# Kernel tuning notes

Hardware: AMD Instinct MI355X
Metric: run time of the kernel (lower is better)

Reference implementation:

```python
import jax, jax.numpy as jnp
import numpy as np

B, T, D, H, L, V = 2, 1024, 768, 12, 6, 32000
HD = D // H
EPS = 1e-5


def _ln(x, w, b):
    mu = jnp.mean(x, axis=-1, keepdims=True)
    var = jnp.mean((x - mu) ** 2, axis=-1, keepdims=True)
    return (x - mu) * jax.lax.rsqrt(var + EPS) * w + b


def setup_inputs() -> dict:
    key = jax.random.key(0)
    ks = jax.random.split(key, 20)
    s = 0.02
    inp = {
        "idx": jax.random.randint(ks[0], (B, T), 0, V),
        "wte": jax.random.normal(ks[1], (V, D), jnp.float32) * s,
        "wpe": jax.random.normal(ks[2], (T, D), jnp.float32) * s,
        # per-layer stacked params (leading dim L)
        "ln1_w": jnp.ones((L, D), jnp.float32),
        "ln1_b": jnp.zeros((L, D), jnp.float32),
        "attn_w": jax.random.normal(ks[3], (L, D, 3 * D), jnp.float32) * s,
        "attn_b": jnp.zeros((L, 3 * D), jnp.float32),
        "proj_w": jax.random.normal(ks[4], (L, D, D), jnp.float32) * s,
        "proj_b": jnp.zeros((L, D), jnp.float32),
        "ln2_w": jnp.ones((L, D), jnp.float32),
        "ln2_b": jnp.zeros((L, D), jnp.float32),
        "fc_w": jax.random.normal(ks[5], (L, D, 4 * D), jnp.float32) * s,
        "fc_b": jnp.zeros((L, 4 * D), jnp.float32),
        "fcproj_w": jax.random.normal(ks[6], (L, 4 * D, D), jnp.float32) * s,
        "fcproj_b": jnp.zeros((L, D), jnp.float32),
        "lnf_w": jnp.ones((D,), jnp.float32),
        "lnf_b": jnp.zeros((D,), jnp.float32),
        "head_w": jax.random.normal(ks[7], (D, V), jnp.float32) * s,
    }
    return inp


def _forward(idx, wte, wpe, ln1_w, ln1_b, attn_w, attn_b, proj_w, proj_b,
             ln2_w, ln2_b, fc_w, fc_b, fcproj_w, fcproj_b, lnf_w, lnf_b, head_w):
    t = idx.shape[1]
    x = wte[idx] + wpe[:t][None]  # [B,T,D]
    causal = jnp.tril(jnp.ones((t, t), bool))
    neg_inf = jnp.asarray(-jnp.inf, x.dtype)
    scale = 1.0 / np.sqrt(HD)

    def block(x, p):
        l1w, l1b, aw, ab, pw, pb, l2w, l2b, fw, fb, fpw, fpb = p
        h = _ln(x, l1w, l1b)
        qkv = h @ aw + ab  # [B,T,3D]
        q, k, v = jnp.split(qkv, 3, axis=-1)
        q = q.reshape(B, t, H, HD).transpose(0, 2, 1, 3)
        k = k.reshape(B, t, H, HD).transpose(0, 2, 1, 3)
        v = v.reshape(B, t, H, HD).transpose(0, 2, 1, 3)
        att = jnp.einsum('bhqd,bhkd->bhqk', q, k) * scale
        att = jnp.where(causal, att, neg_inf)
        att = jax.nn.softmax(att, axis=-1)
        y = jnp.einsum('bhqk,bhkd->bhqd', att, v)
        y = y.transpose(0, 2, 1, 3).reshape(B, t, D) @ pw + pb
        x = x + y
        h2 = _ln(x, l2w, l2b)
        m = jax.nn.gelu(h2 @ fw + fb, approximate=False) @ fpw + fpb
        return x + m, None

    layer_params = (ln1_w, ln1_b, attn_w, attn_b, proj_w, proj_b,
                    ln2_w, ln2_b, fc_w, fc_b, fcproj_w, fcproj_b)
    x, _ = jax.lax.scan(block, x, layer_params)
    logits = _ln(x, lnf_w, lnf_b) @ head_w  # [B,T,V]
    return logits


def reference(idx, wte, wpe, ln1_w, ln1_b, attn_w, attn_b, proj_w, proj_b,
              ln2_w, ln2_b, fc_w, fc_b, fcproj_w, fcproj_b, lnf_w, lnf_b, head_w):
    return _forward(idx, wte, wpe, ln1_w, ln1_b, attn_w, attn_b, proj_w, proj_b,
                    ln2_w, ln2_b, fc_w, fc_b, fcproj_w, fcproj_b, lnf_w, lnf_b, head_w)
```

## Files before the change

kernel.cpp:

```cpp
#include <hip/hip_runtime.h>
#include <hip/hip_bf16.h>
#include <math.h>

static constexpr int Bv = 2, Tv = 1024, Dv = 768, Hv = 12, Lv = 6, Vv = 32000, HDv = 64;
static constexpr int MROWS = Bv * Tv;

typedef __attribute__((ext_vector_type(8))) short bf16x8;
typedef __attribute__((ext_vector_type(8))) short short8;
typedef __attribute__((ext_vector_type(4))) short short4v;
typedef __attribute__((ext_vector_type(4))) float f32x4;

typedef __attribute__((address_space(1))) const void gvoid;
typedef __attribute__((address_space(3))) void svoid;
__device__ __forceinline__ void gld16(const void* g, void* s) {
  __builtin_amdgcn_global_load_lds((gvoid*)g, (svoid*)s, 16, 0, 0);
}
__device__ __forceinline__ short f2bf(float v) {
  __hip_bfloat16 hb = __float2bfloat16(v);
  return *reinterpret_cast<short*>(&hb);
}
__device__ __forceinline__ int xcd_remap(int lin, int nwg) {
  int q = nwg >> 3, r = nwg & 7;
  int xcd = lin & 7, idx = lin >> 3;
  return (xcd < r ? xcd * (q + 1) : r * (q + 1) + (xcd - r) * q) + idx;
}

__global__ __launch_bounds__(256) void embed_kernel(const int* __restrict__ idx,
                                                    const float* __restrict__ wte,
                                                    const float* __restrict__ wpe,
                                                    float* __restrict__ x) {
  int i4 = blockIdx.x * 256 + threadIdx.x;
  int total = MROWS * Dv / 4;
  if (i4 >= total) return;
  int d4 = (i4 % (Dv / 4)) * 4;
  int bt = i4 / (Dv / 4);
  int t  = bt % Tv;
  int id = idx[bt];
  float4 a = *(const float4*)(wte + (size_t)id * Dv + d4);
  float4 p = *(const float4*)(wpe + (size_t)t  * Dv + d4);
  a.x += p.x; a.y += p.y; a.z += p.z; a.w += p.w;
  *(float4*)(x + (size_t)bt * Dv + d4) = a;
}

__global__ __launch_bounds__(256) void ln_kernel(const float* __restrict__ x,
                                                 const float* __restrict__ w,
                                                 const float* __restrict__ b,
                                                 __hip_bfloat16* __restrict__ out) {
  int row = blockIdx.x;
  const float* xr = x + (size_t)row * Dv;
  int tid = threadIdx.x;
  float v0 = xr[tid], v1 = xr[tid + 256], v2 = xr[tid + 512];
  __shared__ float red[8];
  int wid = tid >> 6, lane = tid & 63;

  float s = v0 + v1 + v2;
  #pragma unroll
  for (int off = 1; off < 64; off <<= 1) s += __shfl_xor(s, off, 64);
  if (lane == 0) red[wid] = s;
  __syncthreads();
  s = red[0] + red[1] + red[2] + red[3];
  float mu = s * (1.0f / Dv);

  float d0 = v0 - mu, d1 = v1 - mu, d2 = v2 - mu;
  float q = d0 * d0 + d1 * d1 + d2 * d2;
  #pragma unroll
  for (int off = 1; off < 64; off <<= 1) q += __shfl_xor(q, off, 64);
  if (lane == 0) red[4 + wid] = q;
  __syncthreads();
  q = red[4] + red[5] + red[6] + red[7];
  float rs = rsqrtf(q * (1.0f / Dv) + 1e-5f);

  __hip_bfloat16* orow = out + (size_t)row * Dv;
  orow[tid]       = __float2bfloat16(d0 * rs * w[tid]       + b[tid]);
  orow[tid + 256] = __float2bfloat16(d1 * rs * w[tid + 256] + b[tid + 256]);
  orow[tid + 512] = __float2bfloat16(d2 * rs * w[tid + 512] + b[tid + 512]);
}

__device__ __forceinline__ void tcast_body(const float* __restrict__ W,
                                           __hip_bfloat16* __restrict__ Wt,
                                           int K, int N, int k0, int n0) {
  __shared__ float tile[32][33];
  int tx = threadIdx.x & 31, ty = threadIdx.x >> 5;
  #pragma unroll
  for (int r = 0; r < 32; r += 8)
    tile[ty + r][tx] = W[(size_t)(k0 + ty + r) * N + n0 + tx];
  __syncthreads();
  #pragma unroll
  for (int r = 0; r < 32; r += 8)
    Wt[(size_t)(n0 + ty + r) * K + k0 + tx] = __float2bfloat16(tile[tx][ty + r]);
}

__global__ __launch_bounds__(256) void tcast_kernel(const float* __restrict__ W,
                                                    __hip_bfloat16* __restrict__ Wt,
                                                    int K, int N) {
  tcast_body(W, Wt, K, N, blockIdx.y * 32, blockIdx.x * 32);
}

__global__ __launch_bounds__(256) void tcast4_kernel(const float* __restrict__ s0,
                                                     const float* __restrict__ s1,
                                                     const float* __restrict__ s2,
                                                     const float* __restrict__ s3,
                                                     __hip_bfloat16* __restrict__ d0,
                                                     __hip_bfloat16* __restrict__ d1,
                                                     __hip_bfloat16* __restrict__ d2,
                                                     __hip_bfloat16* __restrict__ d3) {
  int lin = blockIdx.x;
  const float* W; __hip_bfloat16* Wt; int K, N, loc;
  if (lin < 1728)      { W = s0; Wt = d0; K = 768;  N = 2304; loc = lin; }
  else if (lin < 2304) { W = s1; Wt = d1; K = 768;  N = 768;  loc = lin - 1728; }
  else if (lin < 4608) { W = s2; Wt = d2; K = 768;  N = 3072; loc = lin - 2304; }
  else                 { W = s3; Wt = d3; K = 3072; N = 768;  loc = lin - 4608; }
  int nb = N / 32;
  tcast_body(W, Wt, K, N, (loc / nb) * 32, (loc % nb) * 32);
}

template <bool GELU, bool OBF, bool VT>
__device__ __forceinline__ void gemm128_body(const __hip_bfloat16* __restrict__ A,
                                             const __hip_bfloat16* __restrict__ Wt,
                                             const float* __restrict__ bias,
                                             const float* __restrict__ resid,
                                             void* __restrict__ outv,
                                             __hip_bfloat16* __restrict__ vt,
                                             int M, int N, int K) {
  __shared__ short As[2][8192];
  __shared__ short Bs[2][8192];
  int nwg = gridDim.x * gridDim.y;
  int wgid = xcd_remap(blockIdx.y * gridDim.x + blockIdx.x, nwg);
  int m0 = (wgid % gridDim.x) * 128, n0 = (wgid / gridDim.x) * 128;

  int tid = threadIdx.x;
  int w = tid >> 6, lane = tid & 63;
  int wr = w >> 1, wc = w & 1;
  int lr = lane & 15, lk = lane >> 4;

  f32x4 acc[4][4];
  #pragma unroll
  for (int m = 0; m < 4; ++m)
    #pragma unroll
    for (int n = 0; n < 4; ++n) acc[m][n] = (f32x4){0.f, 0.f, 0.f, 0.f};

  auto stg = [&](int k0, int p) {
    #pragma unroll
    for (int e = 0; e < 4; ++e) {
      int idx2 = e * 256 + tid;
      int r = idx2 >> 3, g = idx2 & 7;
      int gs = (g ^ (r & 7)) * 8;
      gld16(A  + (size_t)(m0 + r) * K + k0 + gs, &As[p][idx2 * 8]);
      gld16(Wt + (size_t)(n0 + r) * K + k0 + gs, &Bs[p][idx2 * 8]);
    }
  };

  stg(0, 0);
  __syncthreads();
  int NK = K >> 6;
  for (int kt = 0; kt < NK; ++kt) {
    int p = kt & 1;
    if (kt + 1 < NK) stg((kt + 1) << 6, p ^ 1);
    bf16x8 af[4][2], bf[4][2];
    #pragma unroll
    for (int m = 0; m < 4; ++m) {
      int ra = wr * 64 + m * 16 + lr;
      #pragma unroll
      for (int kf = 0; kf < 2; ++kf)
        af[m][kf] = *(const bf16x8*)(&As[p][ra * 64 + (((kf * 4 + lk) ^ (ra & 7)) * 8)]);
    }
    #pragma unroll
    for (int n = 0; n < 4; ++n) {
      int rb = wc * 64 + n * 16 + lr;
      #pragma unroll
      for (int kf = 0; kf < 2; ++kf)
        bf[n][kf] = *(const bf16x8*)(&Bs[p][rb * 64 + (((kf * 4 + lk) ^ (rb & 7)) * 8)]);
    }
    #pragma unroll
    for (int kf = 0; kf < 2; ++kf)
      #pragma unroll
      for (int m = 0; m < 4; ++m)
        #pragma unroll
        for (int n = 0; n < 4; ++n)
          acc[m][n] = __builtin_amdgcn_mfma_f32_16x16x32_bf16(af[m][kf], bf[n][kf], acc[m][n], 0, 0, 0);
    __syncthreads();
  }

  int row0 = m0 + wr * 64, col0 = n0 + wc * 64;
  float* outf = (float*)outv;
  __hip_bfloat16* outb = (__hip_bfloat16*)outv;
  #pragma unroll
  for (int n = 0; n < 4; ++n) {
    int col = col0 + n * 16 + lr;
    float bv = bias ? bias[col] : 0.f;
    #pragma unroll
    for (int m = 0; m < 4; ++m) {
      int rbase = row0 + m * 16 + lk * 4;
      float r4[4];
      #pragma unroll
      for (int j = 0; j < 4; ++j) {
        float v = acc[m][n][j] + bv;
        if (GELU) v = 0.5f * v * (1.0f + erff(v * 0.70710678118f));
        size_t o = (size_t)(rbase + j) * N + col;
        if (resid) v += resid[o];
        r4[j] = v;
        if (OBF) outb[o] = __float2bfloat16(v);
        else     outf[o] = v;
      }
      if (VT && col >= 2 * Dv) {
        int hh = (col - 2 * Dv) >> 6, dd = (col - 2 * Dv) & 63;
        int bb = rbase >> 10, t0 = rbase & 1023;
        short4v pk = {f2bf(r4[0]), f2bf(r4[1]), f2bf(r4[2]), f2bf(r4[3])};
        *(short4v*)(vt + (((size_t)(bb * Hv + hh) * HDv + dd) << 10) + t0) = pk;
      }
    }
  }
}

__global__ __launch_bounds__(256) void qkv_gemm_kernel(const __hip_bfloat16* A,
                                                       const __hip_bfloat16* Wt,
                                                       const float* bias,
                                                       void* outv, __hip_bfloat16* vt,
                                                       int M, int N, int K) {
  gemm128_body<false, true, true>(A, Wt, bias, nullptr, outv, vt, M, N, K);
}
__global__ __launch_bounds__(256) void fc_gemm_kernel(const __hip_bfloat16* A,
                                                      const __hip_bfloat16* Wt,
                                                      const float* bias,
                                                      void* outv, int M, int N, int K) {
  gemm128_body<true, true, false>(A, Wt, bias, nullptr, outv, nullptr, M, N, K);
}

__device__ __forceinline__ void gemm64_body(const __hip_bfloat16* __restrict__ A,
                                            const __hip_bfloat16* __restrict__ Wt,
                                            const float* __restrict__ bias,
                                            const float* __restrict__ resid,
                                            float* __restrict__ out,
                                            int M, int N, int K) {
  __shared__ short As[2][4096];
  __shared__ short Bs[2][4096];
  int nwg = gridDim.x * gridDim.y;
  int wgid = xcd_remap(blockIdx.y * gridDim.x + blockIdx.x, nwg);
  int m0 = (wgid % gridDim.x) * 64, n0 = (wgid / gridDim.x) * 64;

  int tid = threadIdx.x;
  int w = tid >> 6, lane = tid & 63;
  int wr = w >> 1, wc = w & 1;
  int lr = lane & 15, lk = lane >> 4;
  int rsub = lane >> 3, go = lane & 7;

  f32x4 acc[2][2];
  #pragma unroll
  for (int m = 0; m < 2; ++m)
    #pragma unroll
    for (int n = 0; n < 2; ++n) acc[m][n] = (f32x4){0.f, 0.f, 0.f, 0.f};

  auto stg = [&](int k0, int p) {
    #pragma unroll
    for (int e = 0; e < 2; ++e) {
      int row = w * 16 + e * 8 + rsub;
      int gs = (go ^ rsub) * 8;
      gld16(A  + (size_t)(m0 + row) * K + k0 + gs, &As[p][w * 1024 + e * 512]);
      gld16(Wt + (size_t)(n0 + row) * K + k0 + gs, &Bs[p][w * 1024 + e * 512]);
    }
  };

  stg(0, 0);
  __syncthreads();
  int NK = K >> 6;
  for (int kt = 0; kt < NK; ++kt) {
    int p = kt & 1;
    if (kt + 1 < NK) stg((kt + 1) << 6, p ^ 1);
    #pragma unroll
    for (int kf = 0; kf < 2; ++kf) {
      bf16x8 af[2], bf[2];
      #pragma unroll
      for (int m = 0; m < 2; ++m) {
        int row = wr * 32 + m * 16 + lr;
        af[m] = *(const bf16x8*)(&As[p][row * 64 + (((kf * 4 + lk) ^ (row & 7)) * 8)]);
      }
      #pragma unroll
      for (int n = 0; n < 2; ++n) {
        int row = wc * 32 + n * 16 + lr;
        bf[n] = *(const bf16x8*)(&Bs[p][row * 64 + (((kf * 4 + lk) ^ (row & 7)) * 8)]);
      }
      #pragma unroll
      for (int m = 0; m < 2; ++m)
        #pragma unroll
        for (int n = 0; n < 2; ++n)
          acc[m][n] = __builtin_amdgcn_mfma_f32_16x16x32_bf16(af[m], bf[n], acc[m][n], 0, 0, 0);
    }
    __syncthreads();
  }

  int row0 = m0 + wr * 32, col0 = n0 + wc * 32;
  #pragma unroll
  for (int n = 0; n < 2; ++n) {
    int col = col0 + n * 16 + lr;
    float bv = bias ? bias[col] : 0.f;
    #pragma unroll
    for (int m = 0; m < 2; ++m) {
      int rbase = row0 + m * 16 + lk * 4;
      #pragma unroll
      for (int j = 0; j < 4; ++j) {
        float v = acc[m][n][j] + bv;
        size_t o = (size_t)(rbase + j) * N + col;
        if (resid) v += resid[o];
        out[o] = v;
      }
    }
  }
}

__global__ __launch_bounds__(256) void proj_gemm_kernel(const __hip_bfloat16* A,
                                                        const __hip_bfloat16* Wt,
                                                        const float* bias,
                                                        const float* resid, float* out,
                                                        int M, int N, int K) {
  gemm64_body(A, Wt, bias, resid, out, M, N, K);
}
__global__ __launch_bounds__(256) void fcproj_gemm_kernel(const __hip_bfloat16* A,
                                                          const __hip_bfloat16* Wt,
                                                          const float* bias,
                                                          const float* resid, float* out,
                                                          int M, int N, int K) {
  gemm64_body(A, Wt, bias, resid, out, M, N, K);
}

__global__ __launch_bounds__(512, 2) void gemm256_kernel(const __hip_bfloat16* __restrict__ A,
                                                         const __hip_bfloat16* __restrict__ Wt,
                                                         float* __restrict__ out,
                                                         int N, int K) {
  __shared__ short lds[65536];
  int nwg = gridDim.x * gridDim.y;
  int wgid = xcd_remap(blockIdx.y * gridDim.x + blockIdx.x, nwg);
  int m0 = (wgid % gridDim.x) * 256, n0 = (wgid / gridDim.x) * 256;

  int tid = threadIdx.x;
  int w = tid >> 6, lane = tid & 63;
  int wr = w >> 2, wc = w & 3;
  int lr = lane & 15, lk = lane >> 4;

  f32x4 acc[8][4];
  #pragma unroll
  for (int m = 0; m < 8; ++m)
    #pragma unroll
    for (int n = 0; n < 4; ++n) acc[m][n] = (f32x4){0.f, 0.f, 0.f, 0.f};

  int NT = K >> 6;

  auto stage = [&](int tau, int h) {
    int tsrc = tau < NT ? tau : NT - 1;
    const __hip_bfloat16* mat;
    size_t rb; int lofs;
    if (h == 0)      { mat = A;  rb = (size_t)m0;       lofs = 0; }
    else if (h == 1) { mat = Wt; rb = (size_t)n0;       lofs = 16384; }
    else if (h == 2) { mat = Wt; rb = (size_t)n0 + 128; lofs = 24576; }
    else             { mat = A;  rb = (size_t)m0 + 128; lofs = 8192; }
    short* lb = lds + (tau & 1) * 32768 + lofs;
    #pragma unroll
    for (int e = 0; e < 2; ++e) {
      int idx = e * 512 + tid;
      int r = idx >> 3, g = idx & 7;
      gld16(mat + (rb + r) * (size_t)K + tsrc * 64 + ((g ^ (r & 7)) * 8), lb + idx * 8);
    }
  };

  stage(0, 0); stage(0, 1); stage(0, 2); stage(0, 3);
  asm volatile("s_waitcnt vmcnt(4)" ::: "memory");
  asm volatile("s_barrier" ::: "memory");

  for (int tau = 0; tau < NT; ++tau) {
    const short* bufA = lds + (tau & 1) * 32768;
    const short* bufB = bufA + 16384;
    #pragma unroll
    for (int q = 0; q < 4; ++q) {
      stage(tau + 1, q);
      asm volatile("s_waitcnt vmcnt(4)" ::: "memory");
      int qm = q >> 1, qn = q & 1;
      const short* ab = bufA + qm * 8192;
      const short* bb = bufB + qn * 8192;
      bf16x8 af[4][2], bf[2][2];
      #pragma unroll
      for (int mi = 0; mi < 4; ++mi) {
        int ra = wr * 64 + mi * 16 + lr;
        #pragma unroll
        for (int kf = 0; kf < 2; ++kf)
          af[mi][kf] = *(const bf16x8*)(ab + ra * 64 + (((kf * 4 + lk) ^ (ra & 7)) * 8));
      }
      #pragma unroll
      for (int ni = 0; ni < 2; ++ni) {
        int rb2 = wc * 32 + ni * 16 + lr;
        #pragma unroll
        for (int kf = 0; kf < 2; ++kf)
          bf[ni][kf] = *(const bf16x8*)(bb + rb2 * 64 + (((kf * 4 + lk) ^ (rb2 & 7)) * 8));
      }
      asm volatile("s_barrier" ::: "memory");
      __builtin_amdgcn_s_setprio(1);
      #pragma unroll
      for (int mi = 0; mi < 4; ++mi)
        #pragma unroll
        for (int ni = 0; ni < 2; ++ni)
          #pragma unroll
          for (int kf = 0; kf < 2; ++kf)
            acc[qm * 4 + mi][qn * 2 + ni] = __builtin_amdgcn_mfma_f32_16x16x32_bf16(
                af[mi][kf], bf[ni][kf], acc[qm * 4 + mi][qn * 2 + ni], 0, 0, 0);
      __builtin_amdgcn_s_setprio(0);
      asm volatile("s_barrier" ::: "memory");
    }
  }

  #pragma unroll
  for (int gm = 0; gm < 8; ++gm) {
    int row = m0 + (gm >> 2) * 128 + wr * 64 + (gm & 3) * 16 + lk * 4;
    #pragma unroll
    for (int gn = 0; gn < 4; ++gn) {
      int col = n0 + (gn >> 1) * 128 + wc * 32 + (gn & 1) * 16 + lr;
      #pragma unroll
      for (int j = 0; j < 4; ++j)
        out[(size_t)(row + j) * N + col] = acc[gm][gn][j];
    }
  }
}

__global__ __launch_bounds__(256) void attn_kernel(const __hip_bfloat16* __restrict__ qkv,
                                                   const __hip_bfloat16* __restrict__ vt,
                                                   __hip_bfloat16* __restrict__ y) {
  __shared__ short Ks[2][4096];
  __shared__ short Vts[2][4096];
  __shared__ short Ps[4][1024];
  int b = blockIdx.z, h = blockIdx.y;
  int qb = (gridDim.x - 1 - blockIdx.x) * 64;
  int tid = threadIdx.x;
  int w = tid >> 6, l = tid & 63;
  int lr = l & 15, lk = l >> 4;

  bf16x8 aq[2];
  {
    const __hip_bfloat16* qp = qkv + ((size_t)(b * Tv + qb + w * 16 + lr)) * 3 * Dv + h * HDv + lk * 8;
    aq[0] = *(const bf16x8*)qp;
    aq[1] = *(const bf16x8*)(qp + 32);
  }

  f32x4 o[4];
  #pragma unroll
  for (int n = 0; n < 4; ++n) o[n] = (f32x4){0.f, 0.f, 0.f, 0.f};
  float mrow[4] = {-1e30f, -1e30f, -1e30f, -1e30f};
  float lrow[4] = {0.f, 0.f, 0.f, 0.f};

  int r8 = l >> 3, c8 = l & 7;
  int nt = qb / 64 + 1;

  auto stageKV = [&](int kt2, int p) {
    int kbase = kt2 * 64;
    #pragma unroll
    for (int e = 0; e < 2; ++e) {
      int r0 = w * 16 + e * 8;
      int rK = r0 + r8;
      int csK = c8 ^ (rK & 7);
      gld16(qkv + ((size_t)(b * Tv + kbase + rK)) * 3 * Dv + Dv + h * HDv + csK * 8,
            &Ks[p][r0 * 64]);
      gld16(vt + ((size_t)((b * Hv + h) * HDv + rK)) * Tv + kbase + csK * 8,
            &Vts[p][r0 * 64]);
    }
  };

  stageKV(0, 0);
  __syncthreads();

  for (int kt = 0; kt < nt; ++kt) {
    int p = kt & 1;
    if (kt + 1 < nt) stageKV(kt + 1, p ^ 1);

    f32x4 s[4];
    #pragma unroll
    for (int n = 0; n < 4; ++n) s[n] = (f32x4){0.f, 0.f, 0.f, 0.f};
    __builtin_amdgcn_s_setprio(1);
    #pragma unroll
    for (int kf = 0; kf < 2; ++kf)
      #pragma unroll
      for (int nf = 0; nf < 4; ++nf) {
        int row = nf * 16 + lr;
        int g = (kf * 4 + lk) ^ (row & 7);
        bf16x8 bk = *(const bf16x8*)(&Ks[p][row * 64 + g * 8]);
        s[nf] = __builtin_amdgcn_mfma_f32_16x16x32_bf16(aq[kf], bk, s[nf], 0, 0, 0);
      }
    __builtin_amdgcn_s_setprio(0);
    #pragma unroll
    for (int nf = 0; nf < 4; ++nf)
      #pragma unroll
      for (int j = 0; j < 4; ++j) s[nf][j] *= 0.125f;

    if (kt == nt - 1) {
      #pragma unroll
      for (int nf = 0; nf < 4; ++nf) {
        int kl = nf * 16 + lr;
        #pragma unroll
        for (int j = 0; j < 4; ++j)
          if (kl > w * 16 + lk * 4 + j) s[nf][j] = -1e30f;
      }
    }

    float sc[4];
    #pragma unroll
    for (int j = 0; j < 4; ++j) {
      float pm = fmaxf(fmaxf(s[0][j], s[1][j]), fmaxf(s[2][j], s[3][j]));
      pm = fmaxf(pm, __shfl_xor(pm, 1, 64));
      pm = fmaxf(pm, __shfl_xor(pm, 2, 64));
      pm = fmaxf(pm, __shfl_xor(pm, 4, 64));
      pm = fmaxf(pm, __shfl_xor(pm, 8, 64));
      float mn = fmaxf(mrow[j], pm);
      sc[j] = __expf(mrow[j] - mn);
      mrow[j] = mn;
    }
    #pragma unroll
    for (int j = 0; j < 4; ++j) {
      float ls = 0.f;
      #pragma unroll
      for (int nf = 0; nf < 4; ++nf) {
        float p2 = __expf(s[nf][j] - mrow[j]);
        s[nf][j] = p2;
        ls += p2;
      }
      ls += __shfl_xor(ls, 1, 64);
      ls += __shfl_xor(ls, 2, 64);
      ls += __shfl_xor(ls, 4, 64);
      ls += __shfl_xor(ls, 8, 64);
      lrow[j] = lrow[j] * sc[j] + ls;
    }
    #pragma unroll
    for (int n = 0; n < 4; ++n)
      #pragma unroll
      for (int j = 0; j < 4; ++j) o[n][j] *= sc[j];

    short* pw = Ps[w];
    #pragma unroll
    for (int nf = 0; nf < 4; ++nf)
      #pragma unroll
      for (int j = 0; j < 4; ++j) {
        int ql = lk * 4 + j, k = nf * 16 + lr;
        pw[ql * 64 + (((k >> 3) ^ (ql & 7)) * 8) + (k & 7)] = f2bf(s[nf][j]);
      }
    bf16x8 pa[2];
    #pragma unroll
    for (int kf = 0; kf < 2; ++kf) {
      int g = (kf * 4 + lk) ^ (lr & 7);
      pa[kf] = *(const bf16x8*)(pw + lr * 64 + g * 8);
    }
    __builtin_amdgcn_s_setprio(1);
    #pragma unroll
    for (int kf = 0; kf < 2; ++kf)
      #pragma unroll
      for (int nf = 0; nf < 4; ++nf) {
        int d = nf * 16 + lr;
        int g = (kf * 4 + lk) ^ (d & 7);
        bf16x8 bv = *(const bf16x8*)(&Vts[p][d * 64 + g * 8]);
        o[nf] = __builtin_amdgcn_mfma_f32_16x16x32_bf16(pa[kf], bv, o[nf], 0, 0, 0);
      }
    __builtin_amdgcn_s_setprio(0);
    __syncthreads();
  }

  #pragma unroll
  for (int j = 0; j < 4; ++j) lrow[j] = 1.f / lrow[j];
  #pragma unroll
  for (int nf = 0; nf < 4; ++nf)
    #pragma unroll
    for (int j = 0; j < 4; ++j) {
      size_t oidx = ((size_t)(b * Tv + qb + w * 16 + lk * 4 + j)) * Dv + h * HDv + nf * 16 + lr;
      y[oidx] = __float2bfloat16(o[nf][j] * lrow[j]);
    }
}

extern "C" void kernel_launch(void* const* d_in, const int* in_sizes, int n_in,
                              void* d_out, int out_size, void* d_ws, size_t ws_size,
                              hipStream_t stream) {
  const int*   idx      = (const int*)  d_in[0];
  const float* wte      = (const float*)d_in[1];
  const float* wpe      = (const float*)d_in[2];
  const float* ln1_w    = (const float*)d_in[3];
  const float* ln1_b    = (const float*)d_in[4];
  const float* attn_w   = (const float*)d_in[5];
  const float* attn_b   = (const float*)d_in[6];
  const float* proj_w   = (const float*)d_in[7];
  const float* proj_b   = (const float*)d_in[8];
  const float* ln2_w    = (const float*)d_in[9];
  const float* ln2_b    = (const float*)d_in[10];
  const float* fc_w     = (const float*)d_in[11];
  const float* fc_b     = (const float*)d_in[12];
  const float* fcproj_w = (const float*)d_in[13];
  const float* fcproj_b = (const float*)d_in[14];
  const float* lnf_w    = (const float*)d_in[15];
  const float* lnf_b    = (const float*)d_in[16];
  const float* head_w   = (const float*)d_in[17];
  float* outp = (float*)d_out;

  char* w8 = (char*)d_ws;
  float*          x    = (float*)w8;
  __hip_bfloat16* h    = (__hip_bfloat16*)(w8 + 6291456);
  __hip_bfloat16* qkv  = (__hip_bfloat16*)(w8 + 9437184);
  __hip_bfloat16* m4   = qkv;
  __hip_bfloat16* y    = (__hip_bfloat16*)(w8 + 22020096);
  __hip_bfloat16* vt   = (__hip_bfloat16*)(w8 + 25165824);
  __hip_bfloat16* wbuf = (__hip_bfloat16*)(w8 + 28311552);

  __hip_bfloat16* wb_attn   = wbuf;
  __hip_bfloat16* wb_proj   = wb_attn + (size_t)768 * 2304;
  __hip_bfloat16* wb_fc     = wb_proj + (size_t)768 * 768;
  __hip_bfloat16* wb_fcproj = wb_fc   + (size_t)768 * 3072;

  embed_kernel<<<(MROWS * Dv / 4 + 255) / 256, 256, 0, stream>>>(idx, wte, wpe, x);

  for (int l = 0; l < Lv; ++l) {
    ln_kernel<<<MROWS, 256, 0, stream>>>(x, ln1_w + (size_t)l * Dv, ln1_b + (size_t)l * Dv, h);

    tcast4_kernel<<<6912, 256, 0, stream>>>(
        attn_w   + (size_t)l * Dv * 3 * Dv,
        proj_w   + (size_t)l * Dv * Dv,
        fc_w     + (size_t)l * Dv * 4 * Dv,
        fcproj_w + (size_t)l * 4 * Dv * Dv,
        wb_attn, wb_proj, wb_fc, wb_fcproj);

    qkv_gemm_kernel<<<dim3(MROWS / 128, 3 * Dv / 128), 256, 0, stream>>>(
        h, wb_attn, attn_b + (size_t)l * 3 * Dv, qkv, vt, MROWS, 3 * Dv, Dv);

    attn_kernel<<<dim3(Tv / 64, Hv, Bv), 256, 0, stream>>>(qkv, vt, y);

    proj_gemm_kernel<<<dim3(MROWS / 64, Dv / 64), 256, 0, stream>>>(
        y, wb_proj, proj_b + (size_t)l * Dv, x, x, MROWS, Dv, Dv);

    ln_kernel<<<MROWS, 256, 0, stream>>>(x, ln2_w + (size_t)l * Dv, ln2_b + (size_t)l * Dv, h);

    fc_gemm_kernel<<<dim3(MROWS / 128, 4 * Dv / 128), 256, 0, stream>>>(
        h, wb_fc, fc_b + (size_t)l * 4 * Dv, m4, MROWS, 4 * Dv, Dv);

    fcproj_gemm_kernel<<<dim3(MROWS / 64, Dv / 64), 256, 0, stream>>>(
        m4, wb_fcproj, fcproj_b + (size_t)l * Dv, x, x, MROWS, Dv, 4 * Dv);
  }

  ln_kernel<<<MROWS, 256, 0, stream>>>(x, lnf_w, lnf_b, h);
  tcast_kernel<<<dim3(Vv / 32, Dv / 32), 256, 0, stream>>>(head_w, wbuf, Dv, Vv);
  gemm256_kernel<<<dim3(MROWS / 256, Vv / 256), 512, 0, stream>>>(
      h, wbuf, outp, Vv, Dv);
}
```

Measured before the change: 1.082 ms.

## Batch all weight transposes and embedding into one prestage kernel

When the workspace is large enough, a single prestage kernel fuses the token embedding with bf16 transpose-casts of every layer's weights and the head weight into a per-layer staging area. This removes the seven separate tcast launches from the layer loop and the final head cast. The layer loop then reads per-layer slices of the pre-cast weights. It needs a larger workspace, and it falls back to the old path when the workspace is too small.

```diff
diff --git a/kernel.cpp b/kernel.cpp
--- a/kernel.cpp
+++ b/kernel.cpp
@@ -25,11 +25,11 @@
   return (xcd < r ? xcd * (q + 1) : r * (q + 1) + (xcd - r) * q) + idx;
 }
 
-__global__ __launch_bounds__(256) void embed_kernel(const int* __restrict__ idx,
-                                                    const float* __restrict__ wte,
-                                                    const float* __restrict__ wpe,
-                                                    float* __restrict__ x) {
-  int i4 = blockIdx.x * 256 + threadIdx.x;
+__device__ __forceinline__ void embed_body(const int* __restrict__ idx,
+                                           const float* __restrict__ wte,
+                                           const float* __restrict__ wpe,
+                                           float* __restrict__ x, int blk) {
+  int i4 = blk * 256 + threadIdx.x;
   int total = MROWS * Dv / 4;
   if (i4 >= total) return;
   int d4 = (i4 % (Dv / 4)) * 4;
@@ -40,6 +40,13 @@
   float4 p = *(const float4*)(wpe + (size_t)t  * Dv + d4);
   a.x += p.x; a.y += p.y; a.z += p.z; a.w += p.w;
   *(float4*)(x + (size_t)bt * Dv + d4) = a;
+}
+
+__global__ __launch_bounds__(256) void embed_kernel(const int* __restrict__ idx,
+                                                    const float* __restrict__ wte,
+                                                    const float* __restrict__ wpe,
+                                                    float* __restrict__ x) {
+  embed_body(idx, wte, wpe, x, blockIdx.x);
 }
 
 __global__ __launch_bounds__(256) void ln_kernel(const float* __restrict__ x,
@@ -110,6 +117,44 @@
   else if (lin < 2304) { W = s1; Wt = d1; K = 768;  N = 768;  loc = lin - 1728; }
   else if (lin < 4608) { W = s2; Wt = d2; K = 768;  N = 3072; loc = lin - 2304; }
   else                 { W = s3; Wt = d3; K = 3072; N = 768;  loc = lin - 4608; }
+  int nb = N / 32;
+  tcast_body(W, Wt, K, N, (loc / nb) * 32, (loc % nb) * 32);
+}
+
+__global__ __launch_bounds__(256) void prestage_kernel(const int* __restrict__ idx,
+                                                       const float* __restrict__ wte,
+                                                       const float* __restrict__ wpe,
+                                                       float* __restrict__ x,
+                                                       const float* __restrict__ attn_w,
+                                                       const float* __restrict__ proj_w,
+                                                       const float* __restrict__ fc_w,
+                                                       const float* __restrict__ fcproj_w,
+                                                       const float* __restrict__ head_w,
+                                                       __hip_bfloat16* __restrict__ wb_attn,
+                                                       __hip_bfloat16* __restrict__ wb_proj,
+                                                       __hip_bfloat16* __restrict__ wb_fc,
+                                                       __hip_bfloat16* __restrict__ wb_fcproj,
+                                                       __hip_bfloat16* __restrict__ wb_head) {
+  int lin = blockIdx.x;
+  if (lin < 1536) { embed_body(idx, wte, wpe, x, lin); return; }
+  int t = lin - 1536;
+  const float* W; __hip_bfloat16* Wt; int K, N, loc;
+  if (t < 10368) {
+    int l = t / 1728; loc = t % 1728; K = 768; N = 2304;
+    W = attn_w + (size_t)l * 768 * 2304; Wt = wb_attn + (size_t)l * 768 * 2304;
+  } else if (t < 13824) {
+    int t2 = t - 10368; int l = t2 / 576; loc = t2 % 576; K = 768; N = 768;
+    W = proj_w + (size_t)l * 768 * 768; Wt = wb_proj + (size_t)l * 768 * 768;
+  } else if (t < 27648) {
+    int t3 = t - 13824; int l = t3 / 2304; loc = t3 % 2304; K = 768; N = 3072;
+    W = fc_w + (size_t)l * 768 * 3072; Wt = wb_fc + (size_t)l * 768 * 3072;
+  } else if (t < 41472) {
+    int t4 = t - 27648; int l = t4 / 2304; loc = t4 % 2304; K = 3072; N = 768;
+    W = fcproj_w + (size_t)l * 3072 * 768; Wt = wb_fcproj + (size_t)l * 3072 * 768;
+  } else {
+    loc = t - 41472; K = 768; N = 32000;
+    W = head_w; Wt = wb_head;
+  }
   int nb = N / 32;
   tcast_body(W, Wt, K, N, (loc / nb) * 32, (loc % nb) * 32);
 }
@@ -599,6 +644,38 @@
   __hip_bfloat16* vt   = (__hip_bfloat16*)(w8 + 25165824);
   __hip_bfloat16* wbuf = (__hip_bfloat16*)(w8 + 28311552);
 
+  bool big = ws_size >= 162398208ull;
+  __hip_bfloat16* wa_attn   = wbuf;
+  __hip_bfloat16* wa_proj   = wa_attn   + (size_t)6 * 768 * 2304;
+  __hip_bfloat16* wa_fc     = wa_proj   + (size_t)6 * 768 * 768;
+  __hip_bfloat16* wa_fcproj = wa_fc     + (size_t)6 * 768 * 3072;
+  __hip_bfloat16* wa_head   = wa_fcproj + (size_t)6 * 3072 * 768;
+
+  if (big) {
+    prestage_kernel<<<67008, 256, 0, stream>>>(
+        idx, wte, wpe, x, attn_w, proj_w, fc_w, fcproj_w, head_w,
+        wa_attn, wa_proj, wa_fc, wa_fcproj, wa_head);
+
+    for (int l = 0; l < Lv; ++l) {
+      ln_kernel<<<MROWS, 256, 0, stream>>>(x, ln1_w + (size_t)l * Dv, ln1_b + (size_t)l * Dv, h);
+      qkv_gemm_kernel<<<dim3(MROWS / 128, 3 * Dv / 128), 256, 0, stream>>>(
+          h, wa_attn + (size_t)l * 768 * 2304, attn_b + (size_t)l * 3 * Dv, qkv, vt, MROWS, 3 * Dv, Dv);
+      attn_kernel<<<dim3(Tv / 64, Hv, Bv), 256, 0, stream>>>(qkv, vt, y);
+      proj_gemm_kernel<<<dim3(MROWS / 64, Dv / 64), 256, 0, stream>>>(
+          y, wa_proj + (size_t)l * 768 * 768, proj_b + (size_t)l * Dv, x, x, MROWS, Dv, Dv);
+      ln_kernel<<<MROWS, 256, 0, stream>>>(x, ln2_w + (size_t)l * Dv, ln2_b + (size_t)l * Dv, h);
+      fc_gemm_kernel<<<dim3(MROWS / 128, 4 * Dv / 128), 256, 0, stream>>>(
+          h, wa_fc + (size_t)l * 768 * 3072, fc_b + (size_t)l * 4 * Dv, m4, MROWS, 4 * Dv, Dv);
+      fcproj_gemm_kernel<<<dim3(MROWS / 64, Dv / 64), 256, 0, stream>>>(
+          m4, wa_fcproj + (size_t)l * 3072 * 768, fcproj_b + (size_t)l * Dv, x, x, MROWS, Dv, 4 * Dv);
+    }
+
+    ln_kernel<<<MROWS, 256, 0, stream>>>(x, lnf_w, lnf_b, h);
+    gemm256_kernel<<<dim3(MROWS / 256, Vv / 256), 512, 0, stream>>>(
+        h, wa_head, outp, Vv, Dv);
+    return;
+  }
+
   __hip_bfloat16* wb_attn   = wbuf;
   __hip_bfloat16* wb_proj   = wb_attn + (size_t)768 * 2304;
   __hip_bfloat16* wb_fc     = wb_proj + (size_t)768 * 768;
@@ -608,27 +685,20 @@
 
   for (int l = 0; l < Lv; ++l) {
     ln_kernel<<<MROWS, 256, 0, stream>>>(x, ln1_w + (size_t)l * Dv, ln1_b + (size_t)l * Dv, h);
-
     tcast4_kernel<<<6912, 256, 0, stream>>>(
         attn_w   + (size_t)l * Dv * 3 * Dv,
         proj_w   + (size_t)l * Dv * Dv,
         fc_w     + (size_t)l * Dv * 4 * Dv,
         fcproj_w + (size_t)l * 4 * Dv * Dv,
         wb_attn, wb_proj, wb_fc, wb_fcproj);
-
     qkv_gemm_kernel<<<dim3(MROWS / 128, 3 * Dv / 128), 256, 0, stream>>>(
         h, wb_attn, attn_b + (size_t)l * 3 * Dv, qkv, vt, MROWS, 3 * Dv, Dv);
-
     attn_kernel<<<dim3(Tv / 64, Hv, Bv), 256, 0, stream>>>(qkv, vt, y);
-
     proj_gemm_kernel<<<dim3(MROWS / 64, Dv / 64), 256, 0, stream>>>(
         y, wb_proj, proj_b + (size_t)l * Dv, x, x, MROWS, Dv, Dv);
-
     ln_kernel<<<MROWS, 256, 0, stream>>>(x, ln2_w + (size_t)l * Dv, ln2_b + (size_t)l * Dv, h);
-
     fc_gemm_kernel<<<dim3(MROWS / 128, 4 * Dv / 128), 256, 0, stream>>>(
         h, wb_fc, fc_b + (size_t)l * 4 * Dv, m4, MROWS, 4 * Dv, Dv);
-
     fcproj_gemm_kernel<<<dim3(MROWS / 64, Dv / 64), 256, 0, stream>>>(
         m4, wb_fcproj, fcproj_b + (size_t)l * Dv, x, x, MROWS, Dv, 4 * Dv);
   }
```

Measured after the change: 1.164 ms. +7.6%, slower.
